# Kernel optimization log

Hardware: AMD Instinct MI355X
Metric: run time of the kernel (lower is better)

## Reference

```python
import jax, jax.numpy as jnp
import numpy as np

N = 4096
IN_F = 512
OUT_F = 128
C = 4            # out_channels
ALPHA = 0.2      # leaky relu slope
P_DROP = 0.6
NEG = -9e15


def setup_inputs() -> dict:
    key = jax.random.key(0)
    k1, k2, k3, k4 = jax.random.split(key, 4)
    x = jax.random.normal(k1, (N, IN_F), dtype=jnp.float32)
    # filter-bank output (Chebyshev spectral filter), non-negative-ish values
    attention = jax.random.uniform(k2, (C * N, N), dtype=jnp.float32)
    drop_mask = jax.random.randint(k3, (C * N, N), 0, 2).astype(bool)
    # nn.Linear(in_features, out_features, bias=False): weight [out_f, in_f]
    W = jax.random.normal(k4, (OUT_F, IN_F), dtype=jnp.float32) / np.sqrt(IN_F)
    return {"x": x, "attention": attention, "W": W, "drop_mask": drop_mask}


def reference(x, attention, W, drop_mask):
    h = x @ W.T                                   # [N, out_f]
    n = h.shape[0]
    overall_mean = attention.mean()
    a = jnp.where(attention > overall_mean, attention, jnp.float32(NEG))
    a = jnp.where(a > 0, a, ALPHA * a)            # LeakyReLU
    a = jax.nn.softmax(a, axis=0)                 # softmax over rows (dim=0)
    a = jnp.where(drop_mask, a / (1.0 - P_DROP), 0.0)  # dropout (training)
    h_prime = a @ h                               # [C*N, out_f]
    # concat=True branch: (C, N, F) -> (N, C, F) -> (N, C*F)
    out = h_prime.reshape(C, n, OUT_F).transpose(1, 0, 2).reshape(n, C * OUT_F)
    return out
```

## Files before the change

kernel.cpp:

```cpp
#include <hip/hip_runtime.h>
#include <stdint.h>

#define KDIM  4096
#define NROWS 16384
#define INF   512
#define OUTF  128

typedef short bf16x8 __attribute__((ext_vector_type(8)));
typedef float f32x4  __attribute__((ext_vector_type(4)));
typedef unsigned short u16;

#define WS_MEAN 0
#define WS_RSZ  16
#define WS_H2P  16400
#define WS_W    1064976
#define WS_PART 135282704
#define WS_LEAF WS_PART
#define WS_SUB  (WS_PART + 2097152)
#define WS_ZP   (WS_PART + 2099200)
#define PART_STRIDE ((size_t)NROWS*OUTF)

__device__ __forceinline__ u16 f32_to_bf16_rne(float f){
  unsigned u = __float_as_uint(f);
  unsigned r = u + 0x7fffu + ((u >> 16) & 1u);
  return (u16)(r >> 16);
}

__global__ void __launch_bounds__(256) k_leaf(const float* __restrict__ att,
                                              float* __restrict__ leaf){
  int lf = blockIdx.x*256 + threadIdx.x;
  const float* p = att + (size_t)lf*128;
  float4 u = *(const float4*)p;
  float4 v = *(const float4*)(p + 4);
  float c0=u.x, c1=u.y, c2=u.z, c3=u.w, c4=v.x, c5=v.y, c6=v.z, c7=v.w;
  #pragma unroll
  for (int j = 1; j < 16; ++j){
    float4 a = *(const float4*)(p + j*8);
    float4 b = *(const float4*)(p + j*8 + 4);
    c0+=a.x; c1+=a.y; c2+=a.z; c3+=a.w;
    c4+=b.x; c5+=b.y; c6+=b.z; c7+=b.w;
  }
  leaf[lf] = ((c0+c1)+(c2+c3)) + ((c4+c5)+(c6+c7));
}

__global__ void __launch_bounds__(256) k_tree1(const float* __restrict__ leaf,
                                               float* __restrict__ sub){
  __shared__ float A[1024], B[512];
  int b = blockIdx.x;
  for (int i = threadIdx.x; i < 1024; i += 256) A[i] = leaf[(size_t)b*1024 + i];
  __syncthreads();
  for (int i = threadIdx.x; i < 512; i += 256) B[i] = A[2*i] + A[2*i+1];
  __syncthreads();
  if (threadIdx.x < 256) A[threadIdx.x] = B[2*threadIdx.x] + B[2*threadIdx.x+1];
  __syncthreads();
  int n = 128; float* src = A; float* dst = B;
  while (n >= 1){
    if (threadIdx.x < n) dst[threadIdx.x] = src[2*threadIdx.x] + src[2*threadIdx.x+1];
    __syncthreads();
    float* t = src; src = dst; dst = t; n >>= 1;
  }
  if (threadIdx.x == 0) sub[b] = src[0];
}

__global__ void __launch_bounds__(256) k_tree2(const float* __restrict__ sub,
                                               float* __restrict__ meanv){
  __shared__ float A[512], B[256];
  for (int i = threadIdx.x; i < 512; i += 256) A[i] = sub[i];
  __syncthreads();
  int n = 256; float* src = A; float* dst = B;
  while (n >= 1){
    if (threadIdx.x < n) dst[threadIdx.x] = src[2*threadIdx.x] + src[2*threadIdx.x+1];
    __syncthreads();
    float* t = src; src = dst; dst = t; n >>= 1;
  }
  if (threadIdx.x == 0) meanv[0] = src[0] * (1.0f/67108864.0f);
}

__global__ void __launch_bounds__(256) k_w(const float* __restrict__ att,
                                           const int* __restrict__ mask,
                                           const float* __restrict__ meanv,
                                           u16* __restrict__ w,
                                           float* __restrict__ Zp){
  const float mean = meanv[0];
  const int sb = blockIdx.x & 63;
  const int rs = blockIdx.x >> 6;
  const int c8 = threadIdx.x & 7;
  const int r  = threadIdx.x >> 3;
  const int col = sb*64 + c8*8;
  float a0=0.f,a1=0.f,a2=0.f,a3=0.f,a4=0.f,a5=0.f,a6=0.f,a7=0.f;
  #pragma unroll 2
  for (int it = 0; it < 16; ++it){
    int row = rs*512 + it*32 + r;
    const float* p = att + (size_t)row*KDIM + col;
    const int*   q = mask + (size_t)row*KDIM + col;
    float4 u = *(const float4*)p;
    float4 v = *(const float4*)(p + 4);
    int4 mu = *(const int4*)q;
    int4 mv = *(const int4*)(q + 4);
    float e0 = (u.x > mean) ? __expf(u.x) : 0.f;
    float e1 = (u.y > mean) ? __expf(u.y) : 0.f;
    float e2 = (u.z > mean) ? __expf(u.z) : 0.f;
    float e3 = (u.w > mean) ? __expf(u.w) : 0.f;
    float e4 = (v.x > mean) ? __expf(v.x) : 0.f;
    float e5 = (v.y > mean) ? __expf(v.y) : 0.f;
    float e6 = (v.z > mean) ? __expf(v.z) : 0.f;
    float e7 = (v.w > mean) ? __expf(v.w) : 0.f;
    a0+=e0; a1+=e1; a2+=e2; a3+=e3; a4+=e4; a5+=e5; a6+=e6; a7+=e7;
    bf16x8 wv;
    wv[0]=(short)f32_to_bf16_rne(mu.x ? e0 : 0.f);
    wv[1]=(short)f32_to_bf16_rne(mu.y ? e1 : 0.f);
    wv[2]=(short)f32_to_bf16_rne(mu.z ? e2 : 0.f);
    wv[3]=(short)f32_to_bf16_rne(mu.w ? e3 : 0.f);
    wv[4]=(short)f32_to_bf16_rne(mv.x ? e4 : 0.f);
    wv[5]=(short)f32_to_bf16_rne(mv.y ? e5 : 0.f);
    wv[6]=(short)f32_to_bf16_rne(mv.z ? e6 : 0.f);
    wv[7]=(short)f32_to_bf16_rne(mv.w ? e7 : 0.f);
    *(bf16x8*)(w + (size_t)row*KDIM + col) = wv;
  }
  __shared__ float lds[32][72];
  lds[r][c8*8+0]=a0; lds[r][c8*8+1]=a1; lds[r][c8*8+2]=a2; lds[r][c8*8+3]=a3;
  lds[r][c8*8+4]=a4; lds[r][c8*8+5]=a5; lds[r][c8*8+6]=a6; lds[r][c8*8+7]=a7;
  __syncthreads();
  if (threadIdx.x < 64){
    float s = 0.f;
    #pragma unroll
    for (int rr = 0; rr < 32; ++rr) s += lds[rr][threadIdx.x];
    Zp[(size_t)rs*KDIM + sb*64 + threadIdx.x] = s;
  }
}

__global__ void k_rsz(const float* __restrict__ Zp, float* __restrict__ rsZ){
  int i = blockIdx.x*256 + threadIdx.x;
  if (i < KDIM){
    float s = 0.f;
    #pragma unroll
    for (int rs = 0; rs < 32; ++rs) s += Zp[(size_t)rs*KDIM + i];
    rsZ[i] = 2.5f / s;
  }
}

__device__ __forceinline__ bf16x8 cvt8(float4 a, float4 b){
  bf16x8 r;
  r[0]=(short)f32_to_bf16_rne(a.x); r[1]=(short)f32_to_bf16_rne(a.y);
  r[2]=(short)f32_to_bf16_rne(a.z); r[3]=(short)f32_to_bf16_rne(a.w);
  r[4]=(short)f32_to_bf16_rne(b.x); r[5]=(short)f32_to_bf16_rne(b.y);
  r[6]=(short)f32_to_bf16_rne(b.z); r[7]=(short)f32_to_bf16_rne(b.w);
  return r;
}

__global__ void __launch_bounds__(256) k_h(const float* __restrict__ x,
                                           const float* __restrict__ W,
                                           const float* __restrict__ rsZ,
                                           u16* __restrict__ h2p){
  const int wave = threadIdx.x >> 6, l = threadIdx.x & 63;
  const int rt = blockIdx.x*4 + wave;
  const int m = l & 15, q = l >> 4;
  f32x4 acc[8];
  #pragma unroll
  for (int nt = 0; nt < 8; ++nt) acc[nt] = (f32x4){0.f,0.f,0.f,0.f};
  for (int kb = 0; kb < 16; ++kb){
    const float* xp = x + (size_t)(rt*16+m)*INF + kb*32 + q*8;
    bf16x8 af = cvt8(*(const float4*)xp, *(const float4*)(xp+4));
    #pragma unroll
    for (int nt = 0; nt < 8; ++nt){
      const float* wp = W + (size_t)(nt*16+m)*INF + kb*32 + q*8;
      bf16x8 bf = cvt8(*(const float4*)wp, *(const float4*)(wp+4));
      acc[nt] = __builtin_amdgcn_mfma_f32_16x16x32_bf16(af, bf, acc[nt], 0,0,0);
    }
  }
  float4 rz = *(const float4*)(rsZ + rt*16 + q*4);
  float rzv[4] = {rz.x, rz.y, rz.z, rz.w};
  #pragma unroll
  for (int nt = 0; nt < 8; ++nt)
    #pragma unroll
    for (int r = 0; r < 4; ++r){
      int j = rt*16 + q*4 + r;
      int kb2 = j >> 5, lane_t = ((j>>3)&3)*16 + m, ii = j & 7;
      h2p[(size_t)(kb2*8 + nt)*512 + lane_t*8 + ii] =
          f32_to_bf16_rne(acc[nt][r] * rzv[r]);
    }
}

template<int S>
__global__ void __launch_bounds__(256,2) k_mm(const u16* __restrict__ w,
    const u16* __restrict__ h2p, float* __restrict__ part,
    float* __restrict__ out){
  const int gw = blockIdx.x*4 + (threadIdx.x >> 6);
  const int rp = gw & 511;
  const int kh = gw >> 9;
  const int l = threadIdx.x & 63, m = l & 15, q = l >> 4;
  const int KB = 128 / S;
  const int kb0 = kh * KB;
  const size_t ro0 = (size_t)(rp*32 + m) * KDIM;
  const size_t ro1 = ro0 + (size_t)16 * KDIM;
  f32x4 acc[2][8];
  #pragma unroll
  for (int rt = 0; rt < 2; ++rt)
    #pragma unroll
    for (int nt = 0; nt < 8; ++nt) acc[rt][nt] = (f32x4){0.f,0.f,0.f,0.f};

  bf16x8 Aw0[2], Aw1[2];
  bf16x8 Bv[2][8];

#define LOADSTAGE(kb_, s_) {                                                  \
    const int kc = (kb_)*32 + q*8;                                            \
    Aw0[s_] = *(const bf16x8*)(w + ro0 + kc);                                 \
    Aw1[s_] = *(const bf16x8*)(w + ro1 + kc);                                 \
    const u16* bp_ = h2p + (size_t)((kb_)*8)*512 + l*8;                       \
    _Pragma("unroll")                                                         \
    for (int nt = 0; nt < 8; ++nt) Bv[s_][nt] = *(const bf16x8*)(bp_ + nt*512); }

#define COMPSTAGE(s_) {                                                       \
    _Pragma("unroll")                                                         \
    for (int nt = 0; nt < 8; ++nt){                                           \
      acc[0][nt] = __builtin_amdgcn_mfma_f32_16x16x32_bf16(Aw0[s_], Bv[s_][nt], acc[0][nt], 0,0,0); \
      acc[1][nt] = __builtin_amdgcn_mfma_f32_16x16x32_bf16(Aw1[s_], Bv[s_][nt], acc[1][nt], 0,0,0); } }

  LOADSTAGE(kb0, 0);
  int kb = kb0;
  for (; kb + 2 < kb0 + KB; kb += 2){
    LOADSTAGE(kb+1, 1);
    COMPSTAGE(0);
    LOADSTAGE(kb+2, 0);
    COMPSTAGE(1);
  }
  LOADSTAGE(kb0 + KB - 1, 1);
  COMPSTAGE(0);
  COMPSTAGE(1);
#undef LOADSTAGE
#undef COMPSTAGE

  if (S == 1){
    #pragma unroll
    for (int rt = 0; rt < 2; ++rt)
      #pragma unroll
      for (int nt = 0; nt < 8; ++nt)
        #pragma unroll
        for (int r = 0; r < 4; ++r){
          int i = rp*32 + rt*16 + q*4 + r;
          int f = nt*16 + m;
          out[(size_t)(i & 4095)*512 + (i >> 12)*128 + f] = acc[rt][nt][r];
        }
  } else {
    float* pb = part + (size_t)kh * PART_STRIDE;
    #pragma unroll
    for (int rt = 0; rt < 2; ++rt)
      #pragma unroll
      for (int nt = 0; nt < 8; ++nt)
        #pragma unroll
        for (int r = 0; r < 4; ++r){
          int i = rp*32 + rt*16 + q*4 + r;
          int f = nt*16 + m;
          pb[(size_t)i*128 + f] = acc[rt][nt][r];
        }
  }
}

template<int S>
__global__ void __launch_bounds__(256) k_red(const float* __restrict__ part,
                                             float* __restrict__ out){
  int g = blockIdx.x*256 + threadIdx.x;
  int i = g >> 5;
  int fo = (g & 31) << 2;
  const float* p = part + (size_t)i*128 + fo;
  float4 s = *(const float4*)p;
  #pragma unroll
  for (int kh = 1; kh < S; ++kh){
    float4 t = *(const float4*)(p + (size_t)kh * PART_STRIDE);
    s.x += t.x; s.y += t.y; s.z += t.z; s.w += t.w;
  }
  int n = i & 4095, c = i >> 12;
  *(float4*)(out + (size_t)n*512 + c*128 + fo) = s;
}

extern "C" void kernel_launch(void* const* d_in, const int* in_sizes, int n_in,
                              void* d_out, int out_size, void* d_ws, size_t ws_size,
                              hipStream_t stream) {
  const float* x    = (const float*)d_in[0];
  const float* att  = (const float*)d_in[1];
  const float* W    = (const float*)d_in[2];
  const int*   mask = (const int*)d_in[3];
  float* out = (float*)d_out;

  char* ws = (char*)d_ws;
  float* meanv = (float*)(ws + WS_MEAN);
  float* rsZ   = (float*)(ws + WS_RSZ);
  u16*   h2p   = (u16*)(ws + WS_H2P);
  u16*   wbuf  = (u16*)(ws + WS_W);
  float* part  = (float*)(ws + WS_PART);
  float* leaf  = (float*)(ws + WS_LEAF);
  float* sub   = (float*)(ws + WS_SUB);
  float* Zp    = (float*)(ws + WS_ZP);

  int S = 1;
  if (ws_size >= (size_t)WS_PART + 8ull*PART_STRIDE*4ull) S = 8;
  else if (ws_size >= (size_t)WS_PART + 4ull*PART_STRIDE*4ull) S = 4;

  k_leaf <<<2048, 256, 0, stream>>>(att, leaf);
  k_tree1<<<512,  256, 0, stream>>>(leaf, sub);
  k_tree2<<<1,    256, 0, stream>>>(sub, meanv);
  k_w    <<<2048, 256, 0, stream>>>(att, mask, meanv, wbuf, Zp);
  k_rsz  <<<16,   256, 0, stream>>>(Zp, rsZ);
  k_h    <<<64,   256, 0, stream>>>(x, W, rsZ, h2p);

  switch (S){
    case 8:
      k_mm<8><<<1024, 256, 0, stream>>>(wbuf, h2p, part, out);
      k_red<8><<<2048, 256, 0, stream>>>(part, out);
      break;
    case 4:
      k_mm<4><<<512, 256, 0, stream>>>(wbuf, h2p, part, out);
      k_red<4><<<2048, 256, 0, stream>>>(part, out);
      break;
    default:
      k_mm<1><<<128, 256, 0, stream>>>(wbuf, h2p, part, out);
      break;
  }
}
```

Baseline: 800.3 us.

## Restructure k_w to full-row strips and drop the LDS column reduction

```diff
diff --git a/kernel.cpp b/kernel.cpp
--- a/kernel.cpp
+++ b/kernel.cpp
@@ -17,7 +17,7 @@
 #define WS_PART 135282704
 #define WS_LEAF WS_PART
 #define WS_SUB  (WS_PART + 2097152)
-#define WS_ZP   (WS_PART + 2099200)
+#define WS_ZP   (WS_PART + 4194304)
 #define PART_STRIDE ((size_t)NROWS*OUTF)
 
 __device__ __forceinline__ u16 f32_to_bf16_rne(float f){
@@ -82,61 +82,54 @@
                                            u16* __restrict__ w,
                                            float* __restrict__ Zp){
   const float mean = meanv[0];
-  const int sb = blockIdx.x & 63;
-  const int rs = blockIdx.x >> 6;
-  const int c8 = threadIdx.x & 7;
-  const int r  = threadIdx.x >> 3;
-  const int col = sb*64 + c8*8;
-  float a0=0.f,a1=0.f,a2=0.f,a3=0.f,a4=0.f,a5=0.f,a6=0.f,a7=0.f;
+  const int b = blockIdx.x;
+  const int t = threadIdx.x;
+  float z[16];
+  #pragma unroll
+  for (int i = 0; i < 16; ++i) z[i] = 0.f;
+
   #pragma unroll 2
-  for (int it = 0; it < 16; ++it){
-    int row = rs*512 + it*32 + r;
-    const float* p = att + (size_t)row*KDIM + col;
-    const int*   q = mask + (size_t)row*KDIM + col;
-    float4 u = *(const float4*)p;
-    float4 v = *(const float4*)(p + 4);
-    int4 mu = *(const int4*)q;
-    int4 mv = *(const int4*)(q + 4);
-    float e0 = (u.x > mean) ? __expf(u.x) : 0.f;
-    float e1 = (u.y > mean) ? __expf(u.y) : 0.f;
-    float e2 = (u.z > mean) ? __expf(u.z) : 0.f;
-    float e3 = (u.w > mean) ? __expf(u.w) : 0.f;
-    float e4 = (v.x > mean) ? __expf(v.x) : 0.f;
-    float e5 = (v.y > mean) ? __expf(v.y) : 0.f;
-    float e6 = (v.z > mean) ? __expf(v.z) : 0.f;
-    float e7 = (v.w > mean) ? __expf(v.w) : 0.f;
-    a0+=e0; a1+=e1; a2+=e2; a3+=e3; a4+=e4; a5+=e5; a6+=e6; a7+=e7;
-    bf16x8 wv;
-    wv[0]=(short)f32_to_bf16_rne(mu.x ? e0 : 0.f);
-    wv[1]=(short)f32_to_bf16_rne(mu.y ? e1 : 0.f);
-    wv[2]=(short)f32_to_bf16_rne(mu.z ? e2 : 0.f);
-    wv[3]=(short)f32_to_bf16_rne(mu.w ? e3 : 0.f);
-    wv[4]=(short)f32_to_bf16_rne(mv.x ? e4 : 0.f);
-    wv[5]=(short)f32_to_bf16_rne(mv.y ? e5 : 0.f);
-    wv[6]=(short)f32_to_bf16_rne(mv.z ? e6 : 0.f);
-    wv[7]=(short)f32_to_bf16_rne(mv.w ? e7 : 0.f);
-    *(bf16x8*)(w + (size_t)row*KDIM + col) = wv;
-  }
-  __shared__ float lds[32][72];
-  lds[r][c8*8+0]=a0; lds[r][c8*8+1]=a1; lds[r][c8*8+2]=a2; lds[r][c8*8+3]=a3;
-  lds[r][c8*8+4]=a4; lds[r][c8*8+5]=a5; lds[r][c8*8+6]=a6; lds[r][c8*8+7]=a7;
-  __syncthreads();
-  if (threadIdx.x < 64){
-    float s = 0.f;
-    #pragma unroll
-    for (int rr = 0; rr < 32; ++rr) s += lds[rr][threadIdx.x];
-    Zp[(size_t)rs*KDIM + sb*64 + threadIdx.x] = s;
-  }
-}
-
-__global__ void k_rsz(const float* __restrict__ Zp, float* __restrict__ rsZ){
-  int i = blockIdx.x*256 + threadIdx.x;
-  if (i < KDIM){
-    float s = 0.f;
-    #pragma unroll
-    for (int rs = 0; rs < 32; ++rs) s += Zp[(size_t)rs*KDIM + i];
-    rsZ[i] = 2.5f / s;
-  }
+  for (int r = 0; r < 16; ++r){
+    const size_t ro = ((size_t)b*16 + r) * KDIM;
+    #pragma unroll
+    for (int p = 0; p < 4; ++p){
+      const int c = p*1024 + t*4;
+      float4 u = *(const float4*)(att + ro + c);
+      int4  mu = *(const int4*)(mask + ro + c);
+      float e0 = (u.x > mean) ? __expf(u.x) : 0.f;
+      float e1 = (u.y > mean) ? __expf(u.y) : 0.f;
+      float e2 = (u.z > mean) ? __expf(u.z) : 0.f;
+      float e3 = (u.w > mean) ? __expf(u.w) : 0.f;
+      z[p*4+0]+=e0; z[p*4+1]+=e1; z[p*4+2]+=e2; z[p*4+3]+=e3;
+      ushort4 wv;
+      wv.x = f32_to_bf16_rne(mu.x ? e0 : 0.f);
+      wv.y = f32_to_bf16_rne(mu.y ? e1 : 0.f);
+      wv.z = f32_to_bf16_rne(mu.z ? e2 : 0.f);
+      wv.w = f32_to_bf16_rne(mu.w ? e3 : 0.f);
+      *(ushort4*)(w + ro + c) = wv;
+    }
+  }
+  #pragma unroll
+  for (int p = 0; p < 4; ++p){
+    float4 zv = {z[p*4+0], z[p*4+1], z[p*4+2], z[p*4+3]};
+    *(float4*)(Zp + (size_t)b*KDIM + p*1024 + t*4) = zv;
+  }
+}
+
+__global__ void __launch_bounds__(256) k_rsz(const float* __restrict__ Zp,
+                                             float* __restrict__ rsZ){
+  int col = blockIdx.x*256 + threadIdx.x;
+  float a[16];
+  #pragma unroll
+  for (int i = 0; i < 16; ++i) a[i] = 0.f;
+  for (int bb = 0; bb < 1024; bb += 16){
+    #pragma unroll
+    for (int u = 0; u < 16; ++u)
+      a[u] += Zp[(size_t)(bb+u)*KDIM + col];
+  }
+  float s = (((a[0]+a[1])+(a[2]+a[3])) + ((a[4]+a[5])+(a[6]+a[7])))
+          + (((a[8]+a[9])+(a[10]+a[11])) + ((a[12]+a[13])+(a[14]+a[15])));
+  rsZ[col] = 2.5f / s;
 }
 
 __device__ __forceinline__ bf16x8 cvt8(float4 a, float4 b){
@@ -299,7 +292,7 @@
   k_leaf <<<2048, 256, 0, stream>>>(att, leaf);
   k_tree1<<<512,  256, 0, stream>>>(leaf, sub);
   k_tree2<<<1,    256, 0, stream>>>(sub, meanv);
-  k_w    <<<2048, 256, 0, stream>>>(att, mask, meanv, wbuf, Zp);
+  k_w    <<<1024, 256, 0, stream>>>(att, mask, meanv, wbuf, Zp);
   k_rsz  <<<16,   256, 0, stream>>>(Zp, rsZ);
   k_h    <<<64,   256, 0, stream>>>(x, W, rsZ, h2p);
 
```

New measurement: 792.3 us. Within noise of the previous version (-1.0%).
